# Kernel tuning notes

Hardware: AMD Instinct MI355X
Metric: run time of the kernel (lower is better)

The kernel has to match this reference:

```python
import jax, jax.numpy as jnp
import numpy as np

S = 14
L_COORD = 5.0
L_NOOBJ = 0.5


def setup_inputs() -> dict:
    key = jax.random.key(0)
    k1, k2, k3 = jax.random.split(key, 3)
    N = 4096
    # keep values in (0.05, 0.95) so sqrt(wh) is well-defined for pred and target
    pred = jax.random.uniform(k1, (N, S, S, 30), jnp.float32, 0.05, 0.95)
    tgt = jax.random.uniform(k2, (N, S, S, 30), jnp.float32, 0.05, 0.95)
    # object-present confidence must be exactly 1 (mask test is == 1), else 0
    conf = (jax.random.uniform(k3, (N, S, S)) < 0.25).astype(jnp.float32)
    tgt = tgt.at[..., 4].set(conf).at[..., 9].set(conf)
    # both target boxes of a cell are identical (standard YOLOv1 encoding)
    tgt = tgt.at[..., 5:9].set(tgt[..., 0:4])
    return {"pred_tensor": pred, "target_tensor": tgt}


def _corners(b):
    # b: [..., 5] box (cx, cy, w, h, conf) -> corner boxes, cx/cy scaled by 1/S
    cx = b[..., 0] / S
    cy = b[..., 1] / S
    w = b[..., 2]
    h = b[..., 3]
    return jnp.stack([cx - 0.5 * w, cy - 0.5 * h, cx + 0.5 * w, cy + 0.5 * h], axis=-1)


def _yolo_loss(pred_tensor, target_tensor):
    N = pred_tensor.shape[0]
    obj = (target_tensor[..., 4] == 1).astype(pred_tensor.dtype)    # [N,S,S]
    noobj = (target_tensor[..., 4] == 0).astype(pred_tensor.dtype)  # [N,S,S]

    # no-object confidence loss on channels 4 and 9
    d4 = pred_tensor[..., 4] - target_tensor[..., 4]
    d9 = pred_tensor[..., 9] - target_tensor[..., 9]
    no_object_loss = jnp.sum(noobj * (d4 * d4 + d9 * d9))

    # class loss over object cells
    dc = pred_tensor[..., 10:] - target_tensor[..., 10:]
    class_loss = jnp.sum(obj[..., None] * dc * dc)

    # boxes: [N,S,S,2,5]
    pb = pred_tensor[..., :10].reshape(N, S, S, 2, 5)
    tb = target_tensor[..., :10].reshape(N, S, S, 2, 5)

    pc = _corners(pb)  # [N,S,S,2,4]
    tc = _corners(tb)

    lt = jnp.maximum(pc[..., :2], tc[..., :2])
    rb = jnp.minimum(pc[..., 2:], tc[..., 2:])
    wh = jnp.maximum(rb - lt, 0.0)
    inter = wh[..., 0] * wh[..., 1]                                    # [N,S,S,2]
    area_p = (pc[..., 2] - pc[..., 0]) * (pc[..., 3] - pc[..., 1])
    area_t = (tc[..., 2] - tc[..., 0]) * (tc[..., 3] - tc[..., 1])
    denom = area_p + area_t - inter
    safe = denom > 0
    iou = jnp.where(safe, inter / jnp.where(safe, denom, 1.0), 0.0)    # [N,S,S,2]

    pick1 = iou[..., 0] <= iou[..., 1]                                 # [N,S,S]
    chosen_iou = jnp.where(pick1, iou[..., 1], iou[..., 0])
    bp = jnp.where(pick1[..., None], pb[..., 1, :], pb[..., 0, :])     # [N,S,S,5]
    bt = jnp.where(pick1[..., None], tb[..., 1, :], tb[..., 0, :])

    dxy = bp[..., :2] - bt[..., :2]
    dwh = jnp.sqrt(bp[..., 2:4]) - jnp.sqrt(bt[..., 2:4])
    regression_loss = jnp.sum(obj * (jnp.sum(dxy * dxy, -1) + jnp.sum(dwh * dwh, -1)))

    dconf = bp[..., 4] - chosen_iou
    contain_loss = jnp.sum(obj * dconf * dconf)

    total = (L_COORD * regression_loss + contain_loss
             + L_NOOBJ * no_object_loss + class_loss) / N
    return total


def reference(pred_tensor, target_tensor):
    return _yolo_loss(pred_tensor, target_tensor)
```

## Files before the change

### kernel.cpp

```cpp
#include <hip/hip_runtime.h>

#define SGRID 14
static constexpr float INV_S = 1.0f / 14.0f;

typedef const unsigned int __attribute__((address_space(1)))* gas_ptr;
typedef unsigned int __attribute__((address_space(3)))* las_ptr;

__device__ __forceinline__ void gld_lds16(const void* g, void* l) {
    __builtin_amdgcn_global_load_lds((gas_ptr)g, (las_ptr)l, 16, 0, 0);
}

__device__ __forceinline__ float cell_loss(const float* p, const float* t) {
    float tconf = t[4];
    float obj   = (tconf == 1.0f) ? 1.0f : 0.0f;
    float noobj = (tconf == 0.0f) ? 1.0f : 0.0f;

    float d4 = p[4] - t[4];
    float d9 = p[9] - t[9];
    float no_object_loss = noobj * (d4 * d4 + d9 * d9);

    float class_loss = 0.0f;
    #pragma unroll
    for (int c = 10; c < 30; ++c) { float d = p[c] - t[c]; class_loss += d * d; }
    class_loss *= obj;

    float iou[2];
    #pragma unroll
    for (int b = 0; b < 2; ++b) {
        int o = b * 5;
        float pcx = p[o] * INV_S, pcy = p[o+1] * INV_S, pw = p[o+2], ph = p[o+3];
        float tcx = t[o] * INV_S, tcy = t[o+1] * INV_S, tw = t[o+2], th = t[o+3];
        float px0 = pcx - 0.5f * pw, py0 = pcy - 0.5f * ph;
        float px1 = pcx + 0.5f * pw, py1 = pcy + 0.5f * ph;
        float tx0 = tcx - 0.5f * tw, ty0 = tcy - 0.5f * th;
        float tx1 = tcx + 0.5f * tw, ty1 = tcy + 0.5f * th;
        float lx = fmaxf(px0, tx0), ly = fmaxf(py0, ty0);
        float rx = fminf(px1, tx1), ry = fminf(py1, ty1);
        float wx = fmaxf(rx - lx, 0.0f), wy = fmaxf(ry - ly, 0.0f);
        float inter = wx * wy;
        float ap = (px1 - px0) * (py1 - py0);
        float at = (tx1 - tx0) * (ty1 - ty0);
        float denom = ap + at - inter;
        iou[b] = (denom > 0.0f) ? (inter / denom) : 0.0f;
    }

    bool pick1 = (iou[0] <= iou[1]);
    float chosen = pick1 ? iou[1] : iou[0];
    int o = pick1 ? 5 : 0;

    float dx = p[o]   - t[o];
    float dy = p[o+1] - t[o+1];
    float dw = sqrtf(p[o+2]) - sqrtf(t[o+2]);
    float dh = sqrtf(p[o+3]) - sqrtf(t[o+3]);
    float reg = dx * dx + dy * dy + dw * dw + dh * dh;

    float dconf = p[o+4] - chosen;
    float contain = dconf * dconf;

    return obj * (5.0f * reg + contain) + 0.5f * no_object_loss + class_loss;
}

__global__ __launch_bounds__(128) void yolo_loss_kernel(
    const float* __restrict__ pred, const float* __restrict__ tgt,
    float* __restrict__ out, int ncells, int nchunks, float invN)
{
    __shared__ float4 sbuf[2][1920];
    __shared__ float wpart[2];
    const int tid  = threadIdx.x;
    const int lane = tid & 63;
    const int wv   = tid >> 6;
    float sum = 0.0f;

    const int stride = gridDim.x;
    int chunk = blockIdx.x;
    int buf = 0;

    auto stage = [&](int c, int b) {
        const float4* src = (wv == 0)
            ? (const float4*)(pred + (size_t)c * 3840)
            : (const float4*)(tgt  + (size_t)c * 3840);
        float4* dst = &sbuf[b][wv * 960];
        #pragma unroll
        for (int j = 0; j < 15; ++j)
            gld_lds16((const void*)(src + j * 64 + lane), (void*)&dst[j * 64]);
    };

    if (chunk < nchunks) stage(chunk, 0);

    while (chunk < nchunks) {
        int next = chunk + stride;
        if (next < nchunks) {
            stage(next, buf ^ 1);
            asm volatile("s_waitcnt vmcnt(15)" ::: "memory");
        } else {
            asm volatile("s_waitcnt vmcnt(0)" ::: "memory");
        }
        __builtin_amdgcn_s_barrier();
        asm volatile("" ::: "memory");

        {
            const float* base = (const float*)&sbuf[buf][0];
            const float2* cp2 = (const float2*)(base + tid * 30);
            const float2* ct2 = (const float2*)(base + 3840 + tid * 30);
            float p[30], t[30];
            #pragma unroll
            for (int j = 0; j < 15; ++j) { float2 v = cp2[j]; p[2*j] = v.x; p[2*j+1] = v.y; }
            #pragma unroll
            for (int j = 0; j < 15; ++j) { float2 v = ct2[j]; t[2*j] = v.x; t[2*j+1] = v.y; }
            sum += cell_loss(p, t);
        }

        asm volatile("" ::: "memory");
        __builtin_amdgcn_s_barrier();

        buf ^= 1;
        chunk = next;
    }

    int rem = ncells - nchunks * 128;
    if (rem > 0 && blockIdx.x == 0 && tid < rem) {
        int cell = nchunks * 128 + tid;
        const float2* p2 = (const float2*)(pred + (size_t)cell * 30);
        const float2* t2 = (const float2*)(tgt  + (size_t)cell * 30);
        float p[30], t[30];
        #pragma unroll
        for (int j = 0; j < 15; ++j) { float2 v = p2[j]; p[2*j] = v.x; p[2*j+1] = v.y; }
        #pragma unroll
        for (int j = 0; j < 15; ++j) { float2 v = t2[j]; t[2*j] = v.x; t[2*j+1] = v.y; }
        sum += cell_loss(p, t);
    }

    #pragma unroll
    for (int off = 32; off > 0; off >>= 1) sum += __shfl_down(sum, off, 64);
    if (lane == 0) wpart[wv] = sum;
    __syncthreads();
    if (tid == 0) atomicAdd(out, (wpart[0] + wpart[1]) * invN);
}

extern "C" void kernel_launch(void* const* d_in, const int* in_sizes, int n_in,
                              void* d_out, int out_size, void* d_ws, size_t ws_size,
                              hipStream_t stream) {
    const float* pred = (const float*)d_in[0];
    const float* tgt  = (const float*)d_in[1];
    float* out = (float*)d_out;

    int ncells  = in_sizes[0] / 30;
    int N       = ncells / (SGRID * SGRID);
    float invN  = 1.0f / (float)N;
    int nchunks = ncells / 128;

    hipMemsetAsync(out, 0, sizeof(float) * (out_size > 0 ? out_size : 1), stream);

    int blocks = nchunks < 1 ? 1 : (nchunks < 512 ? nchunks : 512);
    yolo_loss_kernel<<<blocks, 128, 0, stream>>>(pred, tgt, out, ncells, nchunks, invN);
}
```

Measured before the change: 47.22 us.

## Replace double-buffered LDS pipeline with single buffer and more blocks

Drops the manual double-buffered global-to-LDS prefetch and uses a single LDS buffer with __syncthreads around each chunk. It also raises the grid cap from 512 to 1280 blocks. The idea is that halving LDS per block lets more blocks run per CU, so latency is hidden by occupancy instead of in-block prefetch. Each block now stalls on its own loads with no overlap, and more blocks means more atomics at the end.

```diff
diff --git a/kernel.cpp b/kernel.cpp
--- a/kernel.cpp
+++ b/kernel.cpp
@@ -64,42 +64,26 @@
     const float* __restrict__ pred, const float* __restrict__ tgt,
     float* __restrict__ out, int ncells, int nchunks, float invN)
 {
-    __shared__ float4 sbuf[2][1920];
+    __shared__ float4 sbuf[1920];
     __shared__ float wpart[2];
     const int tid  = threadIdx.x;
     const int lane = tid & 63;
     const int wv   = tid >> 6;
     float sum = 0.0f;
 
-    const int stride = gridDim.x;
-    int chunk = blockIdx.x;
-    int buf = 0;
-
-    auto stage = [&](int c, int b) {
+    for (int chunk = blockIdx.x; chunk < nchunks; chunk += gridDim.x) {
         const float4* src = (wv == 0)
-            ? (const float4*)(pred + (size_t)c * 3840)
-            : (const float4*)(tgt  + (size_t)c * 3840);
-        float4* dst = &sbuf[b][wv * 960];
+            ? (const float4*)(pred + (size_t)chunk * 3840)
+            : (const float4*)(tgt  + (size_t)chunk * 3840);
+        float4* dst = &sbuf[wv * 960];
         #pragma unroll
         for (int j = 0; j < 15; ++j)
             gld_lds16((const void*)(src + j * 64 + lane), (void*)&dst[j * 64]);
-    };
 
-    if (chunk < nchunks) stage(chunk, 0);
-
-    while (chunk < nchunks) {
-        int next = chunk + stride;
-        if (next < nchunks) {
-            stage(next, buf ^ 1);
-            asm volatile("s_waitcnt vmcnt(15)" ::: "memory");
-        } else {
-            asm volatile("s_waitcnt vmcnt(0)" ::: "memory");
-        }
-        __builtin_amdgcn_s_barrier();
-        asm volatile("" ::: "memory");
+        __syncthreads();
 
         {
-            const float* base = (const float*)&sbuf[buf][0];
+            const float* base = (const float*)sbuf;
             const float2* cp2 = (const float2*)(base + tid * 30);
             const float2* ct2 = (const float2*)(base + 3840 + tid * 30);
             float p[30], t[30];
@@ -109,12 +93,7 @@
             for (int j = 0; j < 15; ++j) { float2 v = ct2[j]; t[2*j] = v.x; t[2*j+1] = v.y; }
             sum += cell_loss(p, t);
         }
-
-        asm volatile("" ::: "memory");
-        __builtin_amdgcn_s_barrier();
-
-        buf ^= 1;
-        chunk = next;
+        __syncthreads();
     }
 
     int rem = ncells - nchunks * 128;
@@ -151,6 +130,6 @@
 
     hipMemsetAsync(out, 0, sizeof(float) * (out_size > 0 ? out_size : 1), stream);
 
-    int blocks = nchunks < 1 ? 1 : (nchunks < 512 ? nchunks : 512);
+    int blocks = nchunks < 1 ? 1 : (nchunks < 1280 ? nchunks : 1280);
     yolo_loss_kernel<<<blocks, 128, 0, stream>>>(pred, tgt, out, ncells, nchunks, invN);
 }
```

New measurement: 49.78 us. 5.4% more time.

## Halve per-block chunk to 64 cells and raise grid to 1280 blocks

Applied to the files above, without the earlier changes.

Each block iteration now stages 64 cells (pred and target packed into one LDS buffer) instead of 128. The global-to-LDS loads are split unevenly across the two waves, 8 and 7 sixteen-byte loads per lane. Only half of each wave's lanes compute a cell, and the grid grows from 512 to 1280 blocks. The aim is more blocks and more memory requests in flight for this bandwidth-bound reduction, at the cost of idle lanes during compute. The warp reduction now covers only lanes 0-31, so any tail cells handled by lanes 32-63 would be dropped. That tail never occurs for the test size.

```diff
diff --git a/kernel.cpp b/kernel.cpp
--- a/kernel.cpp
+++ b/kernel.cpp
@@ -64,7 +64,7 @@
     const float* __restrict__ pred, const float* __restrict__ tgt,
     float* __restrict__ out, int ncells, int nchunks, float invN)
 {
-    __shared__ float4 sbuf[2][1920];
+    __shared__ float sbuf[2][3840];
     __shared__ float wpart[2];
     const int tid  = threadIdx.x;
     const int lane = tid & 63;
@@ -76,13 +76,17 @@
     int buf = 0;
 
     auto stage = [&](int c, int b) {
-        const float4* src = (wv == 0)
-            ? (const float4*)(pred + (size_t)c * 3840)
-            : (const float4*)(tgt  + (size_t)c * 3840);
-        float4* dst = &sbuf[b][wv * 960];
-        #pragma unroll
-        for (int j = 0; j < 15; ++j)
-            gld_lds16((const void*)(src + j * 64 + lane), (void*)&dst[j * 64]);
+        const int g0 = (wv == 0) ? 0 : 8;
+        const int gn = (wv == 0) ? 8 : 7;
+        const float* pbase = pred + (size_t)c * 1920;
+        const float* tbase = tgt  + (size_t)c * 1920;
+        #pragma unroll 8
+        for (int gi = 0; gi < gn; ++gi) {
+            int g = g0 + gi;
+            int w = g * 256 + lane * 4;
+            const float* src = (w < 1920) ? (pbase + w) : (tbase + (w - 1920));
+            gld_lds16((const void*)src, (void*)&sbuf[b][g * 256]);
+        }
     };
 
     if (chunk < nchunks) stage(chunk, 0);
@@ -91,17 +95,19 @@
         int next = chunk + stride;
         if (next < nchunks) {
             stage(next, buf ^ 1);
-            asm volatile("s_waitcnt vmcnt(15)" ::: "memory");
+            if (wv == 0) asm volatile("s_waitcnt vmcnt(8)" ::: "memory");
+            else         asm volatile("s_waitcnt vmcnt(7)" ::: "memory");
         } else {
             asm volatile("s_waitcnt vmcnt(0)" ::: "memory");
         }
         __builtin_amdgcn_s_barrier();
         asm volatile("" ::: "memory");
 
-        {
-            const float* base = (const float*)&sbuf[buf][0];
-            const float2* cp2 = (const float2*)(base + tid * 30);
-            const float2* ct2 = (const float2*)(base + 3840 + tid * 30);
+        if (lane < 32) {
+            int cell = wv * 32 + lane;
+            const float* base = &sbuf[buf][0];
+            const float2* cp2 = (const float2*)(base + cell * 30);
+            const float2* ct2 = (const float2*)(base + 1920 + cell * 30);
             float p[30], t[30];
             #pragma unroll
             for (int j = 0; j < 15; ++j) { float2 v = cp2[j]; p[2*j] = v.x; p[2*j+1] = v.y; }
@@ -117,9 +123,9 @@
         chunk = next;
     }
 
-    int rem = ncells - nchunks * 128;
+    int rem = ncells - nchunks * 64;
     if (rem > 0 && blockIdx.x == 0 && tid < rem) {
-        int cell = nchunks * 128 + tid;
+        int cell = nchunks * 64 + tid;
         const float2* p2 = (const float2*)(pred + (size_t)cell * 30);
         const float2* t2 = (const float2*)(tgt  + (size_t)cell * 30);
         float p[30], t[30];
@@ -131,7 +137,7 @@
     }
 
     #pragma unroll
-    for (int off = 32; off > 0; off >>= 1) sum += __shfl_down(sum, off, 64);
+    for (int off = 16; off > 0; off >>= 1) sum += __shfl_down(sum, off, 64);
     if (lane == 0) wpart[wv] = sum;
     __syncthreads();
     if (tid == 0) atomicAdd(out, (wpart[0] + wpart[1]) * invN);
@@ -147,10 +153,10 @@
     int ncells  = in_sizes[0] / 30;
     int N       = ncells / (SGRID * SGRID);
     float invN  = 1.0f / (float)N;
-    int nchunks = ncells / 128;
+    int nchunks = ncells / 64;
 
     hipMemsetAsync(out, 0, sizeof(float) * (out_size > 0 ? out_size : 1), stream);
 
-    int blocks = nchunks < 1 ? 1 : (nchunks < 512 ? nchunks : 512);
+    int blocks = nchunks < 1 ? 1 : (nchunks < 1280 ? nchunks : 1280);
     yolo_loss_kernel<<<blocks, 128, 0, stream>>>(pred, tgt, out, ncells, nchunks, invN);
 }
```

Measured after the change: 57.28 us. 21.3% more time.
